# Optimization experiments

Hardware: AMD Instinct MI355X
Metric: run time of the kernel (lower is better)

The kernel has to match this reference:

```python
import jax, jax.numpy as jnp
import numpy as np

QI8_MIN, QI8_MAX = -128.0, 127.0   # torch.qint8 iinfo
QU8_MIN, QU8_MAX = 0.0, 255.0      # torch.quint8 iinfo


def _assym_scale_offset(v, qmin, qmax):
    # mirrors get_tensor_assym_scale_offset: scale=(max-min)/(qmax-qmin), offset=qmin - min/scale
    vmin = v.min()
    vmax = v.max()
    scale = (vmax - vmin) / (qmax - qmin)
    offset = qmin - vmin / scale
    return scale, offset


def _fake_quant(v, scale, zp, qmin, qmax):
    # torch.quantize_per_tensor: q = clamp(round(v/scale + zp), qmin, qmax); dequant = (q - zp)*scale
    q = jnp.clip(jnp.round(v / scale + zp), qmin, qmax)
    return (q - zp) * scale


def setup_inputs() -> dict:
    key = jax.random.key(0)
    k1, k2, k3 = jax.random.split(key, 3)
    x = jax.random.normal(k1, (8192, 4096), jnp.float32)          # quantized activation input (modeled as float)
    weight = jax.random.normal(k2, (4096, 4096), jnp.float32) * 0.02  # Linear.weight [out, in]
    bias = jax.random.normal(k3, (4096,), jnp.float32) * 0.01
    return {"x": x, "weight": weight, "bias": bias}


def reference(x, weight, bias):
    # --- weight quantization (qint8, per-tensor asymmetric, done at __init__) ---
    w_scale, w_off = _assym_scale_offset(weight, QI8_MIN, QI8_MAX)
    w_zp = jnp.round(w_off)  # torch casts zero_point to int
    w_dq = _fake_quant(weight, w_scale, w_zp, QI8_MIN, QI8_MAX)

    # --- input is a quint8 quantized tensor; model quantize->dequantize ---
    x_scale, x_off = _assym_scale_offset(x, QU8_MIN, QU8_MAX)
    x_zp = jnp.round(x_off)
    x_dq = _fake_quant(x, x_scale, x_zp, QU8_MIN, QU8_MAX)

    # --- calibration pass (not _computed): float Linear on dequantized input ---
    act = x_dq @ weight.T + bias                 # [tokens, out]
    a_scale, a_off = _assym_scale_offset(act, QU8_MIN, QU8_MAX)
    a_zp = jnp.round(a_off)

    # --- qF.linear: int8 GEMM (dequantized form) + bias, requantized to quint8 ---
    out = x_dq @ w_dq.T + bias
    return _fake_quant(out, a_scale, a_zp, QU8_MIN, QU8_MAX)
```

## Files before the change

### kernel.cpp

```cpp
#include <hip/hip_runtime.h>
#include <stdint.h>

#define M_DIM 8192
#define N_DIM 4096
#define K_DIM 4096

typedef __attribute__((ext_vector_type(4))) int i32x4;

__device__ __forceinline__ unsigned fkey(float f) {
  unsigned u = __float_as_uint(f);
  return (u & 0x80000000u) ? ~u : (u | 0x80000000u);
}
__device__ __forceinline__ float finv(unsigned k) {
  return __uint_as_float((k & 0x80000000u) ? (k ^ 0x80000000u) : ~k);
}
__device__ __forceinline__ void async16(const void* g, void* l) {
  __builtin_amdgcn_global_load_lds(
      (const __attribute__((address_space(1))) void*)g,
      (__attribute__((address_space(3))) void*)l, 16, 0, 0);
}

__global__ void minmax_fused(const float* __restrict__ x, const float* __restrict__ w,
                             unsigned* __restrict__ stats) {
  const bool isX = blockIdx.x < 2048;
  const float4* v4 = isX ? (const float4*)x : (const float4*)w;
  const int n4 = isX ? (M_DIM * K_DIM / 4) : (N_DIM * K_DIM / 4);
  const int bid = isX ? blockIdx.x : (blockIdx.x - 2048);
  const int nb = isX ? 2048 : 1024;
  int i0 = bid * blockDim.x + threadIdx.x;
  int stride = nb * blockDim.x;
  float vmin = 3.4e38f, vmax = -3.4e38f;
  for (int i = i0; i < n4; i += stride) {
    float4 t = v4[i];
    vmin = fminf(vmin, fminf(fminf(t.x, t.y), fminf(t.z, t.w)));
    vmax = fmaxf(vmax, fmaxf(fmaxf(t.x, t.y), fmaxf(t.z, t.w)));
  }
  unsigned kmin = fkey(vmin), kmax = ~fkey(vmax);
  #pragma unroll
  for (int off = 32; off; off >>= 1) {
    unsigned t0 = __shfl_down(kmin, (unsigned)off, 64);
    unsigned t1 = __shfl_down(kmax, (unsigned)off, 64);
    kmin = kmin < t0 ? kmin : t0;
    kmax = kmax < t1 ? kmax : t1;
  }
  if ((threadIdx.x & 63) == 0) {
    int base = isX ? 0 : 2;
    atomicMin(&stats[base + 0], kmin);
    atomicMin(&stats[base + 1], kmax);
  }
}

__global__ void quant_fused(const float* __restrict__ x, const float* __restrict__ w,
                            const unsigned* __restrict__ stats,
                            signed char* __restrict__ A8, signed char* __restrict__ B8,
                            signed char* __restrict__ R8,
                            int* __restrict__ rowA, int* __restrict__ colB, int* __restrict__ colR) {
  __shared__ int sr[8];
  const int tid = threadIdx.x;
  const int lane = tid & 63;
  const int wv = tid >> 6;
  if (blockIdx.x < M_DIM) {
    const int row = blockIdx.x;
    const float xmin = finv(stats[0]), xmax = finv(~stats[1]);
    const float xs = (xmax - xmin) / 255.0f;
    const float xzp = rintf(0.0f - xmin / xs);
    const float4* xr = (const float4*)(x + (size_t)row * K_DIM);
    char4* ar = (char4*)(A8 + (size_t)row * K_DIM);
    int s = 0;
    #pragma unroll
    for (int i = 0; i < 4; ++i) {
      int idx = tid + i * 256;
      float4 t = xr[idx];
      int q0 = (int)(fminf(fmaxf(rintf(t.x / xs + xzp), 0.f), 255.f)) - 128;
      int q1 = (int)(fminf(fmaxf(rintf(t.y / xs + xzp), 0.f), 255.f)) - 128;
      int q2 = (int)(fminf(fmaxf(rintf(t.z / xs + xzp), 0.f), 255.f)) - 128;
      int q3 = (int)(fminf(fmaxf(rintf(t.w / xs + xzp), 0.f), 255.f)) - 128;
      char4 c4; c4.x = (signed char)q0; c4.y = (signed char)q1;
      c4.z = (signed char)q2; c4.w = (signed char)q3;
      ar[idx] = c4;
      s += q0 + q1 + q2 + q3;
    }
    #pragma unroll
    for (int off = 32; off; off >>= 1) s += __shfl_down(s, (unsigned)off, 64);
    if (lane == 0) sr[wv] = s;
    __syncthreads();
    if (tid == 0) rowA[row] = sr[0] + sr[1] + sr[2] + sr[3];
  } else {
    const int row = blockIdx.x - M_DIM;
    const float wmin = finv(stats[2]), wmax = finv(~stats[3]);
    const float ws = (wmax - wmin) / 255.0f;
    const float wzp = rintf(-128.0f - wmin / ws);
    const float inv_rs = 126.0f / ws;
    const float4* wr = (const float4*)(w + (size_t)row * K_DIM);
    char4* br = (char4*)(B8 + (size_t)row * K_DIM);
    char4* rr = (char4*)(R8 + (size_t)row * K_DIM);
    int sb = 0, srr = 0;
    #pragma unroll
    for (int i = 0; i < 4; ++i) {
      int idx = tid + i * 256;
      float4 t = wr[idx];
      char4 bq, rq;
      float v, qf; int q, r;
      v = t.x; qf = fminf(fmaxf(rintf(v / ws + wzp), -128.f), 127.f); q = (int)qf;
      r = (int)fminf(fmaxf(rintf((v - ws * (qf - wzp)) * inv_rs), -127.f), 127.f);
      bq.x = (signed char)q; rq.x = (signed char)r; sb += q; srr += r;
      v = t.y; qf = fminf(fmaxf(rintf(v / ws + wzp), -128.f), 127.f); q = (int)qf;
      r = (int)fminf(fmaxf(rintf((v - ws * (qf - wzp)) * inv_rs), -127.f), 127.f);
      bq.y = (signed char)q; rq.y = (signed char)r; sb += q; srr += r;
      v = t.z; qf = fminf(fmaxf(rintf(v / ws + wzp), -128.f), 127.f); q = (int)qf;
      r = (int)fminf(fmaxf(rintf((v - ws * (qf - wzp)) * inv_rs), -127.f), 127.f);
      bq.z = (signed char)q; rq.z = (signed char)r; sb += q; srr += r;
      v = t.w; qf = fminf(fmaxf(rintf(v / ws + wzp), -128.f), 127.f); q = (int)qf;
      r = (int)fminf(fmaxf(rintf((v - ws * (qf - wzp)) * inv_rs), -127.f), 127.f);
      bq.w = (signed char)q; rq.w = (signed char)r; sb += q; srr += r;
      br[idx] = bq; rr[idx] = rq;
    }
    #pragma unroll
    for (int off = 32; off; off >>= 1) {
      sb += __shfl_down(sb, (unsigned)off, 64);
      srr += __shfl_down(srr, (unsigned)off, 64);
    }
    if (lane == 0) { sr[wv] = sb; sr[4 + wv] = srr; }
    __syncthreads();
    if (tid == 0) {
      colB[row] = sr[0] + sr[1] + sr[2] + sr[3];
      colR[row] = sr[4] + sr[5] + sr[6] + sr[7];
    }
  }
}

__global__ __launch_bounds__(512, 4) void gemm_i8(
    const signed char* __restrict__ A8, const signed char* __restrict__ B8,
    const signed char* __restrict__ R8,
    const int* __restrict__ rowA, const int* __restrict__ colB, const int* __restrict__ colR,
    const float* __restrict__ bias, unsigned* __restrict__ stats,
    float* __restrict__ outp) {
  __shared__ __align__(16) signed char sA[128 * 64];
  __shared__ __align__(16) signed char sB[128 * 64];
  __shared__ __align__(16) signed char sR[128 * 64];
  __shared__ unsigned s_red[2];

  const int tid = threadIdx.x;
  const int wave = tid >> 6;
  const int lane = tid & 63;
  const int xcd = blockIdx.x & 7;
  const int s = blockIdx.x >> 3;
  const int bn = xcd * 4 + (s >> 6);
  const int bm = s & 63;
  const int rowBase = bm * 128;
  const int colBase = bn * 128;
  const int wr = wave >> 2;
  const int wc = wave & 3;
  const int laneR = lane & 15;
  const int laneK = (lane >> 4) * 16;

  if (tid == 0) { s_red[0] = 0xFFFFFFFFu; s_red[1] = 0xFFFFFFFFu; }

  i32x4 acc_q[4][2];
  i32x4 acc_r[4][2];
  const i32x4 zero = {0, 0, 0, 0};
  #pragma unroll
  for (int i = 0; i < 4; ++i) { acc_q[i][0] = zero; acc_q[i][1] = zero;
                                acc_r[i][0] = zero; acc_r[i][1] = zero; }

  const signed char* srcA = A8 + (size_t)(rowBase + wave * 16 + laneR) * K_DIM + laneK;
  const signed char* srcB = B8 + (size_t)(colBase + wave * 16 + laneR) * K_DIM + laneK;
  const signed char* srcR = R8 + (size_t)(colBase + wave * 16 + laneR) * K_DIM + laneK;
  signed char* dA = sA + wave * 1024 + lane * 16;
  signed char* dB = sB + wave * 1024 + lane * 16;
  signed char* dR = sR + wave * 1024 + lane * 16;

  for (int kt = 0; kt < K_DIM; kt += 64) {
    async16(srcA + kt, dA);
    async16(srcB + kt, dB);
    async16(srcR + kt, dR);
    __syncthreads();

    i32x4 af[4];
    #pragma unroll
    for (int mi = 0; mi < 4; ++mi)
      af[mi] = *(const i32x4*)(sA + (wr * 4 + mi) * 1024 + lane * 16);
    #pragma unroll
    for (int ni = 0; ni < 2; ++ni) {
      const int bo = (wc * 2 + ni) * 1024 + lane * 16;
      i32x4 bf = *(const i32x4*)(sB + bo);
      i32x4 rf = *(const i32x4*)(sR + bo);
      #pragma unroll
      for (int mi = 0; mi < 4; ++mi) {
        acc_q[mi][ni] = __builtin_amdgcn_mfma_i32_16x16x64_i8(af[mi], bf, acc_q[mi][ni], 0, 0, 0);
        acc_r[mi][ni] = __builtin_amdgcn_mfma_i32_16x16x64_i8(af[mi], rf, acc_r[mi][ni], 0, 0, 0);
      }
    }
    __syncthreads();
  }

  const float xmin = finv(stats[0]), xmax = finv(~stats[1]);
  const float xs = (xmax - xmin) / 255.0f;
  const float xzp = rintf(0.0f - xmin / xs);
  const float wmin = finv(stats[2]), wmax = finv(~stats[3]);
  const float ws = (wmax - wmin) / 255.0f;
  const float wzp = rintf(-128.0f - wmin / ws);
  const int c = 128 - (int)xzp;
  const int wzpi = (int)wzp;
  const float sw = xs * ws;
  const float xrs = xs * (ws / 126.0f);
  const int ccK = c * wzpi * K_DIM;
  unsigned kmin = 0xFFFFFFFFu, kmax = 0xFFFFFFFFu;

  int rAv[4][4];
  #pragma unroll
  for (int mi = 0; mi < 4; ++mi) {
    const int row0 = rowBase + wr * 64 + mi * 16 + (lane >> 4) * 4;
    #pragma unroll
    for (int r = 0; r < 4; ++r) rAv[mi][r] = rowA[row0 + r];
  }

  #pragma unroll
  for (int ni = 0; ni < 2; ++ni) {
    const int col = colBase + wc * 32 + ni * 16 + laneR;
    const float bv = bias[col];
    const int base_n = c * colB[col] - ccK;
    const int cR = c * colR[col];
    #pragma unroll
    for (int mi = 0; mi < 4; ++mi) {
      const int row0 = rowBase + wr * 64 + mi * 16 + (lane >> 4) * 4;
      #pragma unroll
      for (int r = 0; r < 4; ++r) {
        const int S = acc_q[mi][ni][r] + base_n - wzpi * rAv[mi][r];
        const float ov = sw * (float)S + bv;
        const int S2 = acc_r[mi][ni][r] + cR;
        const float av = ov + xrs * (float)S2;
        const unsigned k = fkey(av);
        const unsigned kf = ~k;
        kmin = kmin < k ? kmin : k;
        kmax = kmax < kf ? kmax : kf;
        outp[(size_t)(row0 + r) * N_DIM + col] = ov;
      }
    }
  }

  #pragma unroll
  for (int off = 32; off; off >>= 1) {
    unsigned t0 = __shfl_down(kmin, (unsigned)off, 64);
    unsigned t1 = __shfl_down(kmax, (unsigned)off, 64);
    kmin = kmin < t0 ? kmin : t0;
    kmax = kmax < t1 ? kmax : t1;
  }
  __syncthreads();
  if (lane == 0) { atomicMin(&s_red[0], kmin); atomicMin(&s_red[1], kmax); }
  __syncthreads();
  if (tid == 0) { atomicMin(&stats[4], s_red[0]); atomicMin(&stats[5], s_red[1]); }
}

__global__ void requant_kernel(float* __restrict__ out, const unsigned* __restrict__ stats, int n4) {
  const float amin = finv(stats[4]), amax = finv(~stats[5]);
  const float as = (amax - amin) / 255.0f;
  const float azp = rintf(0.0f - amin / as);
  float4* o4 = (float4*)out;
  int i0 = blockIdx.x * blockDim.x + threadIdx.x;
  int stride = gridDim.x * blockDim.x;
  for (int i = i0; i < n4; i += stride) {
    float4 t = o4[i];
    t.x = (fminf(fmaxf(rintf(t.x / as + azp), 0.f), 255.f) - azp) * as;
    t.y = (fminf(fmaxf(rintf(t.y / as + azp), 0.f), 255.f) - azp) * as;
    t.z = (fminf(fmaxf(rintf(t.z / as + azp), 0.f), 255.f) - azp) * as;
    t.w = (fminf(fmaxf(rintf(t.w / as + azp), 0.f), 255.f) - azp) * as;
    o4[i] = t;
  }
}

extern "C" void kernel_launch(void* const* d_in, const int* in_sizes, int n_in,
                              void* d_out, int out_size, void* d_ws, size_t ws_size,
                              hipStream_t stream) {
  const float* x = (const float*)d_in[0];
  const float* w = (const float*)d_in[1];
  const float* bias = (const float*)d_in[2];
  float* out = (float*)d_out;

  unsigned* stats = (unsigned*)d_ws;
  signed char* A8 = (signed char*)d_ws + 256;
  signed char* B8 = A8 + (size_t)M_DIM * K_DIM;
  signed char* R8 = B8 + (size_t)N_DIM * K_DIM;
  int* rowA = (int*)(R8 + (size_t)N_DIM * K_DIM);
  int* colB = rowA + M_DIM;
  int* colR = colB + N_DIM;

  hipMemsetAsync(stats, 0xFF, 24, stream);
  minmax_fused<<<3072, 256, 0, stream>>>(x, w, stats);
  quant_fused<<<M_DIM + N_DIM, 256, 0, stream>>>(x, w, stats, A8, B8, R8, rowA, colB, colR);
  gemm_i8<<<(M_DIM / 128) * (N_DIM / 128), 512, 0, stream>>>(A8, B8, R8, rowA, colB, colR, bias, stats, out);
  requant_kernel<<<2048, 256, 0, stream>>>(out, stats, M_DIM * N_DIM / 4);
}
```

Baseline: 989.6 us.

## Double-buffer LDS tiles in int8 GEMM to overlap loads with MFMA

Doubles the shared-memory buffers for the A, B and residual int8 tiles and restructures the K loop so the async global-to-LDS load of the next tile is issued before computing the current one. This is meant to hide global memory latency behind the MFMA work and halve the number of barrier stalls spent waiting on loads. LDS use grows from 24KB to 48KB per block, which may reduce the number of resident blocks per CU below what the launch bounds request.

```diff
diff --git a/kernel.cpp b/kernel.cpp
--- a/kernel.cpp
+++ b/kernel.cpp
@@ -135,9 +135,9 @@
     const int* __restrict__ rowA, const int* __restrict__ colB, const int* __restrict__ colR,
     const float* __restrict__ bias, unsigned* __restrict__ stats,
     float* __restrict__ outp) {
-  __shared__ __align__(16) signed char sA[128 * 64];
-  __shared__ __align__(16) signed char sB[128 * 64];
-  __shared__ __align__(16) signed char sR[128 * 64];
+  __shared__ __align__(16) signed char sA[2 * 128 * 64];
+  __shared__ __align__(16) signed char sB[2 * 128 * 64];
+  __shared__ __align__(16) signed char sR[2 * 128 * 64];
   __shared__ unsigned s_red[2];
 
   const int tid = threadIdx.x;
@@ -170,29 +170,48 @@
   signed char* dB = sB + wave * 1024 + lane * 16;
   signed char* dR = sR + wave * 1024 + lane * 16;
 
-  for (int kt = 0; kt < K_DIM; kt += 64) {
-    async16(srcA + kt, dA);
-    async16(srcB + kt, dB);
-    async16(srcR + kt, dR);
+#define STAGE(b, kt) do {                        \
+    async16(srcA + (kt), dA + (b) * 8192);       \
+    async16(srcB + (kt), dB + (b) * 8192);       \
+    async16(srcR + (kt), dR + (b) * 8192);       \
+  } while (0)
+
+#define COMPUTE(b) do {                                                        \
+    i32x4 af[4];                                                               \
+    _Pragma("unroll")                                                          \
+    for (int mi = 0; mi < 4; ++mi)                                             \
+      af[mi] = *(const i32x4*)(sA + (b) * 8192 + (wr * 4 + mi) * 1024 + lane * 16); \
+    _Pragma("unroll")                                                          \
+    for (int ni = 0; ni < 2; ++ni) {                                           \
+      const int bo = (b) * 8192 + (wc * 2 + ni) * 1024 + lane * 16;            \
+      i32x4 bf = *(const i32x4*)(sB + bo);                                     \
+      i32x4 rf = *(const i32x4*)(sR + bo);                                     \
+      _Pragma("unroll")                                                        \
+      for (int mi = 0; mi < 4; ++mi) {                                         \
+        acc_q[mi][ni] = __builtin_amdgcn_mfma_i32_16x16x64_i8(af[mi], bf, acc_q[mi][ni], 0, 0, 0); \
+        acc_r[mi][ni] = __builtin_amdgcn_mfma_i32_16x16x64_i8(af[mi], rf, acc_r[mi][ni], 0, 0, 0); \
+      }                                                                        \
+    }                                                                          \
+  } while (0)
+
+  STAGE(0, 0);
+  __syncthreads();
+
+  for (int kt = 0; kt < K_DIM - 128; kt += 128) {
+    STAGE(1, kt + 64);
+    COMPUTE(0);
     __syncthreads();
-
-    i32x4 af[4];
-    #pragma unroll
-    for (int mi = 0; mi < 4; ++mi)
-      af[mi] = *(const i32x4*)(sA + (wr * 4 + mi) * 1024 + lane * 16);
-    #pragma unroll
-    for (int ni = 0; ni < 2; ++ni) {
-      const int bo = (wc * 2 + ni) * 1024 + lane * 16;
-      i32x4 bf = *(const i32x4*)(sB + bo);
-      i32x4 rf = *(const i32x4*)(sR + bo);
-      #pragma unroll
-      for (int mi = 0; mi < 4; ++mi) {
-        acc_q[mi][ni] = __builtin_amdgcn_mfma_i32_16x16x64_i8(af[mi], bf, acc_q[mi][ni], 0, 0, 0);
-        acc_r[mi][ni] = __builtin_amdgcn_mfma_i32_16x16x64_i8(af[mi], rf, acc_r[mi][ni], 0, 0, 0);
-      }
-    }
+    STAGE(0, kt + 128);
+    COMPUTE(1);
     __syncthreads();
   }
+  STAGE(1, K_DIM - 64);
+  COMPUTE(0);
+  __syncthreads();
+  COMPUTE(1);
+
+#undef STAGE
+#undef COMPUTE
 
   const float xmin = finv(stats[0]), xmax = finv(~stats[1]);
   const float xs = (xmax - xmin) / 255.0f;
```

Result: no change. 980.6 us (-0.9%).
